# Kernel tuning notes

Measured on AMD Instinct MI355X. Metric: run time of the kernel, lower is better.

## Reference

```python
import jax, jax.numpy as jnp
from jax import lax
import numpy as np

TAG_NAMES = ["O", "B-MAT", "I-MAT", "B-PRO", "I-PRO", "B-APL", "I-APL", "B-SMT", "I-SMT", "B-CMT", "I-CMT", "B-DSC", "I-DSC"]
IMP = -100.0


def _init_crf_params(key):
    # torchcrf initializes uniform(-0.1, 0.1); CRF_NEW then clamps invalid
    # BIO transitions to -100 per define_invalid_crf_transitions/init_crf_transitions.
    K = len(TAG_NAMES)
    k1, k2, k3 = jax.random.split(key, 3)
    start = np.array(jax.random.uniform(k1, (K,), minval=-0.1, maxval=0.1), dtype=np.float32)
    end = np.array(jax.random.uniform(k2, (K,), minval=-0.1, maxval=0.1), dtype=np.float32)
    trans = np.array(jax.random.uniform(k3, (K, K), minval=-0.1, maxval=0.1), dtype=np.float32)
    pref = [t[0] for t in TAG_NAMES]
    ent = [t.split('-')[1] if '-' in t else '' for t in TAG_NAMES]
    for i in range(K):
        if pref[i] in ('B', 'I'):  # invalid begin/end for BIO
            start[i] = IMP
            end[i] = IMP
    for i in range(K):
        for j in range(K):
            # invalid_transitions_position: O -> I  (B->P, I->P are empty sets)
            if pref[i] == 'O' and pref[j] == 'I':
                trans[i, j] = IMP
            # invalid_transitions_tags: B->I, I->I across different entity types
            if pref[i] in ('B', 'I') and pref[j] == 'I' and ent[i] != ent[j]:
                trans[i, j] = IMP
    return jnp.asarray(start), jnp.asarray(end), jnp.asarray(trans)


def setup_inputs() -> dict:
    key = jax.random.key(0)
    k_em, k_tag, k_p = jax.random.split(key, 3)
    B, T, K = 4096, 512, len(TAG_NAMES)
    emissions = jax.random.normal(k_em, (B, T, K), dtype=jnp.float32)
    tags = jax.random.randint(k_tag, (B, T), 0, K, dtype=jnp.int64)
    mask = jnp.ones((B, T), dtype=bool)
    start_transitions, end_transitions, transitions = _init_crf_params(k_p)
    return {"emissions": emissions, "tags": tags, "mask": mask,
            "start_transitions": start_transitions,
            "end_transitions": end_transitions,
            "transitions": transitions}


def reference(emissions, tags, mask, start_transitions, end_transitions, transitions):
    # torchcrf CRF.forward with batch_first=True, reduction='sum':
    # returns sum over batch of log p(tags | emissions).
    B, T, K = emissions.shape
    maskf = mask.astype(emissions.dtype)

    # ---- numerator: score of the given tag path ----
    emit = jnp.take_along_axis(emissions, tags[..., None], axis=2)[..., 0]  # [B,T]
    trans = transitions[tags[:, :-1], tags[:, 1:]]                           # [B,T-1]
    num = start_transitions[tags[:, 0]] + emit[:, 0]
    num = num + jnp.sum((trans + emit[:, 1:]) * maskf[:, 1:], axis=1)
    seq_ends = jnp.sum(mask.astype(jnp.int32), axis=1) - 1                   # [B]
    last_tags = tags[jnp.arange(B), seq_ends]
    num = num + end_transitions[last_tags]

    # ---- denominator: log partition via forward-algorithm scan over time ----
    em_t = jnp.swapaxes(emissions, 0, 1)   # [T,B,K]
    mask_t = jnp.swapaxes(mask, 0, 1)      # [T,B]
    score0 = start_transitions + em_t[0]   # [B,K]

    def step(score, xs):
        em, m = xs  # em: [B,K], m: [B]
        # broadcast: [B,K_from,1] + [K_from,K_to] + [B,1,K_to]
        nxt = jax.nn.logsumexp(score[:, :, None] + transitions[None] + em[:, None, :], axis=1)
        return jnp.where(m[:, None], nxt, score), None

    score, _ = lax.scan(step, score0, (em_t[1:], mask_t[1:]))
    denom = jax.nn.logsumexp(score + end_transitions, axis=1)  # [B]

    return jnp.sum(num - denom)
```

## Files before the change

kernel.cpp:

```cpp
#include <hip/hip_runtime.h>


typedef float  f4  __attribute__((ext_vector_type(4)));
typedef short  s4  __attribute__((ext_vector_type(4)));
typedef int    i2  __attribute__((ext_vector_type(2)));

__device__ __forceinline__ unsigned pack_bf16(float x, float y) {
  return __builtin_amdgcn_perm(__float_as_uint(y) + 0x8000u,
                               __float_as_uint(x) + 0x8000u, 0x07060302u);
}

__device__ __forceinline__ void gll16(const void* g, void* l) {
  __builtin_amdgcn_global_load_lds(
      (const __attribute__((address_space(1))) void*)g,
      (__attribute__((address_space(3))) void*)l, 16, 0, 0);
}

#define VMWAIT(N) do { asm volatile("s_waitcnt vmcnt(" #N ")" ::: "memory"); \
                       __builtin_amdgcn_sched_barrier(0); } while (0)
#define SB0() __builtin_amdgcn_sched_barrier(0)

__global__ void __launch_bounds__(128, 1)
crf_main(const float* __restrict__ em,
         const int*   __restrict__ tags,
         const float* __restrict__ startT,
         const float* __restrict__ endT,
         const float* __restrict__ trans,
         float* __restrict__ partial)
{
  __shared__ __align__(16) float emST[2][3][4096];
  __shared__ __align__(16) int   tagST[2][3][256];
  __shared__ float ldsT[256];
  __shared__ float ldsS[16], ldsE[16];
  __shared__ float pFa[256];
  __shared__ float lsF[16], numF[16], resB[16];
  __shared__ int   tag255[16];

  const int tid = threadIdx.x;
  for (int i = tid; i < 169; i += 128) {
    const int r_ = i / 13, c_ = i - r_ * 13;
    ldsT[r_ * 16 + c_] = trans[i];
  }
  if (tid < 13) ldsS[tid] = startT[tid];
  if (tid >= 16 && tid < 29) ldsE[tid - 16] = endT[tid - 16];
  __syncthreads();

  const int lane = tid & 63;
  const int n    = lane & 15;
  const int q    = lane >> 4;
  const bool is_fwd = (tid < 64);
  const int  w   = is_fwd ? 0 : 1;
  const int  seq = blockIdx.x * 16 + n;
  const int loadBase = (q < 3) ? 4 * q : 9;
  const int lo       = (q < 3) ? 4 * q : 12;
  const unsigned span = (q < 3) ? 3u : 0u;
  const float* emL = em   + (size_t)seq * 6656 + loadBase;
  const int*   tgL = tags + (size_t)seq * 512 + 4 * q;
  const int   lofs = lane * 4;

  s4 afrag;
  {
    float av[4];
#pragma unroll
    for (int i = 0; i < 4; ++i) {
      const int kk = 4 * q + i;
      av[i] = (kk < 13 && n < 13)
            ? __expf(is_fwd ? ldsT[kk * 16 + n] : ldsT[n * 16 + kk]) : 0.0f;
    }
    i2 ai = { (int)pack_bf16(av[0], av[1]), (int)pack_bf16(av[2], av[3]) };
    afrag = __builtin_bit_cast(s4, ai);
  }

  f4 D;
#pragma unroll
  for (int r = 0; r < 4; ++r) {
    const int m = 4 * q + r;
    D[r] = (m < 13) ? __expf(is_fwd ? ldsS[m] : ldsE[m]) : 0.0f;
  }

  float logscale = 0.0f, em_acc = 0.0f, trans_acc = 0.0f;
  float sDs0 = 0, sDs1 = 0, sDs2 = 0, sDs3 = 0;
  float start_t0 = 0.0f;
  int tg_hi = 0, tg_lo = 0, tg511 = 0;
  int4 tG[4];

#define TGV(k) ((((k) & 3) == 0) ? tG[(k) >> 2].x : (((k) & 3) == 1) ? tG[(k) >> 2].y \
              : (((k) & 3) == 2) ? tG[(k) >> 2].z : tG[(k) >> 2].w)

#define STAGE(SL, TC) do {                                               \
    float* eb_ = &emST[w][SL][0];                                        \
    const float* gp_ = emL + (size_t)(TC) * 13;                          \
    _Pragma("unroll")                                                    \
    for (int k_ = 0; k_ < 16; ++k_)                                      \
      gll16(gp_ + (size_t)k_ * 13, eb_ + k_ * 256);                      \
    gll16(tgL + (TC), &tagST[w][SL][0]);                                 \
  } while (0)

#define LDTAGS(SL) do {                                                  \
    _Pragma("unroll")                                                    \
    for (int g_ = 0; g_ < 4; ++g_)                                       \
      tG[g_] = *(const int4*)&tagST[w][SL][(g_ * 16 + n) * 4];           \
  } while (0)

#define RENORM4() do {                                                  \
    float cm_ = fmaxf(fmaxf(Ds0, Ds1), fmaxf(Ds2, Ds3));                \
    cm_ = fmaxf(cm_, __shfl_xor(cm_, 16, 64));                          \
    cm_ = fmaxf(cm_, __shfl_xor(cm_, 32, 64));                          \
    const float rc_ = __builtin_amdgcn_rcpf(cm_);                       \
    Ds0 *= rc_; Ds1 *= rc_; Ds2 *= rc_; Ds3 *= rc_;                     \
    logscale += __logf(cm_);                                            \
  } while (0)

#define CORE(EM4, RN, TGVv) do {                                        \
    const float e0 = __expf((q == 3) ? (EM4).w : (EM4).x);              \
    const float e1 = __expf((EM4).y);                                   \
    const float e2 = __expf((EM4).z);                                   \
    const float e3 = __expf((EM4).w);                                   \
    Ds0 = D[0] * e0; Ds1 = D[1] * e1; Ds2 = D[2] * e2; Ds3 = D[3] * e3; \
    if (RN) RENORM4();                                                  \
    {                                                                   \
      const unsigned ur_ = (unsigned)((TGVv) - lo);                     \
      const int rr_ = (TGVv) - loadBase;                                \
      const float s01_ = (rr_ & 1) ? (EM4).y : (EM4).x;                 \
      const float s23_ = (rr_ & 1) ? (EM4).w : (EM4).z;                 \
      const float sv_  = (rr_ & 2) ? s23_ : s01_;                       \
      em_acc += (ur_ <= span) ? sv_ : 0.0f;                             \
    }                                                                   \
    {                                                                   \
      i2 bi_ = { (int)pack_bf16(Ds0, Ds1), (int)pack_bf16(Ds2, Ds3) };  \
      s4 bf_ = __builtin_bit_cast(s4, bi_);                             \
      D = __builtin_amdgcn_mfma_f32_16x16x16bf16_1k(                    \
              afrag, bf_, (f4){0.f, 0.f, 0.f, 0.f}, 0, 0, 0);           \
    }                                                                   \
  } while (0)

#define PROCF(SL, FIRST, LAST) do {                                     \
    _Pragma("unroll")                                                   \
    for (int k = 0; k < 16; ++k) {                                      \
      const int tgv = TGV(k);                                           \
      if (FIRST && k == 0) start_t0 = ldsS[tgv];                        \
      else {                                                            \
        const int pv = (k == 0) ? tg_hi : TGV(k - 1);                   \
        trans_acc += ldsT[pv * 16 + tgv];                               \
      }                                                                 \
      const f4 em4 = *(const f4*)&emST[w][SL][k * 256 + lofs];          \
      float Ds0, Ds1, Ds2, Ds3;                                         \
      CORE(em4, (k == 7 || k == 15), tgv);                              \
      if (LAST && k == 15) { sDs0 = Ds0; sDs1 = Ds1; sDs2 = Ds2; sDs3 = Ds3; } \
    }                                                                   \
    tg_hi = TGV(15);                                                    \
  } while (0)

#define PROCB(SL, FIRST) do {                                           \
    if (FIRST) tg511 = TGV(15);                                         \
    else       trans_acc += ldsT[TGV(15) * 16 + tg_lo];                 \
    _Pragma("unroll")                                                   \
    for (int kk = 0; kk < 16; ++kk) {                                   \
      const int k = 15 - kk;                                            \
      const int tgv = TGV(k);                                           \
      if (k > 0) trans_acc += ldsT[TGV(k - 1) * 16 + tgv];              \
      const f4 em4 = *(const f4*)&emST[w][SL][k * 256 + lofs];          \
      float Ds0, Ds1, Ds2, Ds3;                                         \
      CORE(em4, (k == 8 || k == 0), tgv);                               \
    }                                                                   \
    tg_lo = TGV(0);                                                     \
  } while (0)

  if (is_fwd) {
    STAGE(0, 0); STAGE(1, 16); STAGE(2, 32);
    VMWAIT(34); LDTAGS(0); PROCF(0, true, false); SB0(); STAGE(0, 48);
#pragma unroll 1
    for (int c = 1; c <= 10; c += 3) {
      VMWAIT(34); LDTAGS(1); PROCF(1, false, false); SB0(); STAGE(1, 16 * c + 48);
      VMWAIT(34); LDTAGS(2); PROCF(2, false, false); SB0(); STAGE(2, 16 * c + 64);
      VMWAIT(34); LDTAGS(0); PROCF(0, false, false); SB0(); STAGE(0, 16 * c + 80);
    }
    VMWAIT(34); LDTAGS(1); PROCF(1, false, false);
    VMWAIT(17); LDTAGS(2); PROCF(2, false, false);
    VMWAIT(0);  LDTAGS(0); PROCF(0, false, true);
    float emr = em_acc + __shfl_xor(em_acc, 16, 64);
    emr += __shfl_xor(emr, 32, 64);
    if (q == 0) {
      lsF[n]    = logscale;
      numF[n]   = start_t0 + emr + trans_acc;
      tag255[n] = tg_hi;
    }
    *(f4*)&pFa[n * 16 + 4 * q] = (f4){sDs0, sDs1, sDs2, sDs3};
  } else {
    STAGE(0, 496); STAGE(1, 480); STAGE(2, 464);
    VMWAIT(34); LDTAGS(0); PROCB(0, true); SB0(); STAGE(0, 448);
#pragma unroll 1
    for (int c = 1; c <= 10; c += 3) {
      VMWAIT(34); LDTAGS(1); PROCB(1, false); SB0(); STAGE(1, 448 - 16 * c);
      VMWAIT(34); LDTAGS(2); PROCB(2, false); SB0(); STAGE(2, 432 - 16 * c);
      VMWAIT(34); LDTAGS(0); PROCB(0, false); SB0(); STAGE(0, 416 - 16 * c);
    }
    VMWAIT(34); LDTAGS(1); PROCB(1, false);
    VMWAIT(17); LDTAGS(2); PROCB(2, false);
    VMWAIT(0);  LDTAGS(0); PROCB(0, false);
  }

  __syncthreads();

  if (!is_fwd) {
    const f4 al = *(const f4*)&pFa[n * 16 + 4 * q];
    float z = al[0] * D[0] + al[1] * D[1] + al[2] * D[2] + al[3] * D[3];
    z += __shfl_xor(z, 16, 64);
    z += __shfl_xor(z, 32, 64);
    float emr = em_acc + __shfl_xor(em_acc, 16, 64);
    emr += __shfl_xor(emr, 32, 64);
    const float denom = lsF[n] + logscale + __logf(z);
    const float num   = numF[n] + emr + trans_acc
                      + ldsT[tag255[n] * 16 + tg_lo]
                      + ldsE[tg511];
    if (q == 0) resB[n] = num - denom;
  }
  __syncthreads();
  if (tid == 0) {
    float s = 0.0f;
#pragma unroll
    for (int i = 0; i < 16; ++i) s += resB[i];
    partial[blockIdx.x] = s;
  }

#undef TGV
#undef STAGE
#undef LDTAGS
#undef RENORM4
#undef CORE
#undef PROCF
#undef PROCB
}

__global__ void __launch_bounds__(256)
crf_reduce(const float* __restrict__ part, float* __restrict__ out, int n)
{
  float v = 0.0f;
  for (int i = threadIdx.x; i < n; i += 256) v += part[i];
#pragma unroll
  for (int off = 32; off > 0; off >>= 1) v += __shfl_down(v, off);
  __shared__ float w[4];
  if ((threadIdx.x & 63) == 0) w[threadIdx.x >> 6] = v;
  __syncthreads();
  if (threadIdx.x == 0) out[0] = (w[0] + w[1]) + (w[2] + w[3]);
}

extern "C" void kernel_launch(void* const* d_in, const int* in_sizes, int n_in,
                              void* d_out, int out_size, void* d_ws, size_t ws_size,
                              hipStream_t stream) {
  const float* em   = (const float*)d_in[0];
  const int*   tags = (const int*)d_in[1];
  const float* st   = (const float*)d_in[3];
  const float* en   = (const float*)d_in[4];
  const float* tr   = (const float*)d_in[5];
  float* part = (float*)d_ws;

  crf_main<<<256, 128, 0, stream>>>(em, tags, st, en, tr, part);
  crf_reduce<<<1, 256, 0, stream>>>(part, (float*)d_out, 256);
}
```

Baseline: 194.3 us.

## Split batch into smaller blocks of four sequences with register-staged chunk loads

Each block now handles 4 sequences instead of 16 and the grid grows fourfold, with launch bounds allowing two blocks per CU. The aim is more resident waves per CU to hide the latency of the serial forward/backward recurrence. Emissions and tags now come in as 32-step chunks through registers into a double-buffered LDS area, replacing the triple-buffered direct global-to-LDS loads. The 16-column MFMA now holds each sequence four times, so per-sequence math is redundant. LDS emission reads become scalar with a 13-float stride.

```diff
diff --git a/kernel.cpp b/kernel.cpp
--- a/kernel.cpp
+++ b/kernel.cpp
@@ -5,22 +5,14 @@
 typedef short  s4  __attribute__((ext_vector_type(4)));
 typedef int    i2  __attribute__((ext_vector_type(2)));
 
+#define SB0() __builtin_amdgcn_sched_barrier(0)
+
 __device__ __forceinline__ unsigned pack_bf16(float x, float y) {
   return __builtin_amdgcn_perm(__float_as_uint(y) + 0x8000u,
                                __float_as_uint(x) + 0x8000u, 0x07060302u);
 }
 
-__device__ __forceinline__ void gll16(const void* g, void* l) {
-  __builtin_amdgcn_global_load_lds(
-      (const __attribute__((address_space(1))) void*)g,
-      (__attribute__((address_space(3))) void*)l, 16, 0, 0);
-}
-
-#define VMWAIT(N) do { asm volatile("s_waitcnt vmcnt(" #N ")" ::: "memory"); \
-                       __builtin_amdgcn_sched_barrier(0); } while (0)
-#define SB0() __builtin_amdgcn_sched_barrier(0)
-
-__global__ void __launch_bounds__(128, 1)
+__global__ void __launch_bounds__(128, 2)
 crf_main(const float* __restrict__ em,
          const int*   __restrict__ tags,
          const float* __restrict__ startT,
@@ -28,12 +20,12 @@
          const float* __restrict__ trans,
          float* __restrict__ partial)
 {
-  __shared__ __align__(16) float emST[2][3][4096];
-  __shared__ __align__(16) int   tagST[2][3][256];
+  __shared__ __align__(16) float emLds[2][2][4 * 420];
+  __shared__ __align__(16) int   tgLds[2][2][4 * 36];
   __shared__ float ldsT[256];
   __shared__ float ldsS[16], ldsE[16];
   __shared__ float pFa[256];
-  __shared__ float lsF[16], numF[16], resB[16];
+  __shared__ float lsF[16], numF[16], resB[4];
   __shared__ int   tag255[16];
 
   const int tid = threadIdx.x;
@@ -50,13 +42,19 @@
   const int q    = lane >> 4;
   const bool is_fwd = (tid < 64);
   const int  w   = is_fwd ? 0 : 1;
-  const int  seq = blockIdx.x * 16 + n;
+  const int  sl  = n & 3;
   const int loadBase = (q < 3) ? 4 * q : 9;
   const int lo       = (q < 3) ? 4 * q : 12;
   const unsigned span = (q < 3) ? 3u : 0u;
-  const float* emL = em   + (size_t)seq * 6656 + loadBase;
-  const int*   tgL = tags + (size_t)seq * 512 + 4 * q;
-  const int   lofs = lane * 4;
+  const int lb = loadBase;
+
+  const int ls = lane >> 4;
+  const int lp = lane & 15;
+  const int ts   = lane >> 3;
+  const int tg_g = lane & 7;
+  const int seqBlock = blockIdx.x * 4;
+  const float* emBase = em   + (size_t)(seqBlock + ls) * 6656;
+  const int*   tgBase = tags + (size_t)(seqBlock + ts) * 512;
 
   s4 afrag;
   {
@@ -82,24 +80,35 @@
   float sDs0 = 0, sDs1 = 0, sDs2 = 0, sDs3 = 0;
   float start_t0 = 0.0f;
   int tg_hi = 0, tg_lo = 0, tg511 = 0;
-  int4 tG[4];
+  int4 tG[8];
+  f4   rr[7];
+  int4 rt;
 
 #define TGV(k) ((((k) & 3) == 0) ? tG[(k) >> 2].x : (((k) & 3) == 1) ? tG[(k) >> 2].y \
               : (((k) & 3) == 2) ? tG[(k) >> 2].z : tG[(k) >> 2].w)
 
-#define STAGE(SL, TC) do {                                               \
-    float* eb_ = &emST[w][SL][0];                                        \
-    const float* gp_ = emL + (size_t)(TC) * 13;                          \
-    _Pragma("unroll")                                                    \
-    for (int k_ = 0; k_ < 16; ++k_)                                      \
-      gll16(gp_ + (size_t)k_ * 13, eb_ + k_ * 256);                      \
-    gll16(tgL + (TC), &tagST[w][SL][0]);                                 \
-  } while (0)
-
-#define LDTAGS(SL) do {                                                  \
-    _Pragma("unroll")                                                    \
-    for (int g_ = 0; g_ < 4; ++g_)                                       \
-      tG[g_] = *(const int4*)&tagST[w][SL][(g_ * 16 + n) * 4];           \
+#define LOADCH(T0) do {                                                 \
+    const float* gb_ = emBase + (size_t)(T0) * 13;                      \
+    _Pragma("unroll")                                                   \
+    for (int j_ = 0; j_ < 6; ++j_)                                      \
+      rr[j_] = *(const f4*)(gb_ + j_ * 64 + lp * 4);                    \
+    if (lp < 8) rr[6] = *(const f4*)(gb_ + 384 + lp * 4);               \
+    if (lane < 32) rt = *(const int4*)(tgBase + (T0) + tg_g * 4);       \
+  } while (0)
+
+#define WRCH(SL) do {                                                   \
+    float* wb_ = &emLds[w][SL][ls * 420];                               \
+    _Pragma("unroll")                                                   \
+    for (int j_ = 0; j_ < 6; ++j_)                                      \
+      *(f4*)(wb_ + j_ * 64 + lp * 4) = rr[j_];                          \
+    if (lp < 8) *(f4*)(wb_ + 384 + lp * 4) = rr[6];                     \
+    if (lane < 32) *(int4*)&tgLds[w][SL][ts * 36 + tg_g * 4] = rt;      \
+  } while (0)
+
+#define LDTAGS(SL) do {                                                 \
+    _Pragma("unroll")                                                   \
+    for (int g_ = 0; g_ < 8; ++g_)                                      \
+      tG[g_] = *(const int4*)&tgLds[w][SL][sl * 36 + g_ * 4];           \
   } while (0)
 
 #define RENORM4() do {                                                  \
@@ -134,50 +143,56 @@
     }                                                                   \
   } while (0)
 
+#define EMRD(SL, k, EM4) do {                                           \
+    const float* eb_ = &emLds[w][SL][sl * 420 + lb];                    \
+    (EM4).x = eb_[(k) * 13];     (EM4).y = eb_[(k) * 13 + 1];           \
+    (EM4).z = eb_[(k) * 13 + 2]; (EM4).w = eb_[(k) * 13 + 3];           \
+  } while (0)
+
 #define PROCF(SL, FIRST, LAST) do {                                     \
     _Pragma("unroll")                                                   \
-    for (int k = 0; k < 16; ++k) {                                      \
+    for (int k = 0; k < 32; ++k) {                                      \
       const int tgv = TGV(k);                                           \
-      if (FIRST && k == 0) start_t0 = ldsS[tgv];                        \
+      if ((FIRST) && k == 0) start_t0 = ldsS[tgv];                      \
       else {                                                            \
         const int pv = (k == 0) ? tg_hi : TGV(k - 1);                   \
         trans_acc += ldsT[pv * 16 + tgv];                               \
       }                                                                 \
-      const f4 em4 = *(const f4*)&emST[w][SL][k * 256 + lofs];          \
+      f4 em4; EMRD(SL, k, em4);                                         \
       float Ds0, Ds1, Ds2, Ds3;                                         \
-      CORE(em4, (k == 7 || k == 15), tgv);                              \
-      if (LAST && k == 15) { sDs0 = Ds0; sDs1 = Ds1; sDs2 = Ds2; sDs3 = Ds3; } \
-    }                                                                   \
-    tg_hi = TGV(15);                                                    \
+      CORE(em4, ((k & 7) == 7), tgv);                                   \
+      if ((LAST) && k == 31) { sDs0 = Ds0; sDs1 = Ds1; sDs2 = Ds2; sDs3 = Ds3; } \
+    }                                                                   \
+    tg_hi = TGV(31);                                                    \
   } while (0)
 
 #define PROCB(SL, FIRST) do {                                           \
-    if (FIRST) tg511 = TGV(15);                                         \
-    else       trans_acc += ldsT[TGV(15) * 16 + tg_lo];                 \
-    _Pragma("unroll")                                                   \
-    for (int kk = 0; kk < 16; ++kk) {                                   \
-      const int k = 15 - kk;                                            \
+    if (FIRST) tg511 = TGV(31);                                         \
+    else       trans_acc += ldsT[TGV(31) * 16 + tg_lo];                 \
+    _Pragma("unroll")                                                   \
+    for (int kk = 0; kk < 32; ++kk) {                                   \
+      const int k = 31 - kk;                                            \
       const int tgv = TGV(k);                                           \
       if (k > 0) trans_acc += ldsT[TGV(k - 1) * 16 + tgv];              \
-      const f4 em4 = *(const f4*)&emST[w][SL][k * 256 + lofs];          \
+      f4 em4; EMRD(SL, k, em4);                                         \
       float Ds0, Ds1, Ds2, Ds3;                                         \
-      CORE(em4, (k == 8 || k == 0), tgv);                               \
+      CORE(em4, ((k & 7) == 0), tgv);                                   \
     }                                                                   \
     tg_lo = TGV(0);                                                     \
   } while (0)
 
   if (is_fwd) {
-    STAGE(0, 0); STAGE(1, 16); STAGE(2, 32);
-    VMWAIT(34); LDTAGS(0); PROCF(0, true, false); SB0(); STAGE(0, 48);
+    LOADCH(0); SB0(); WRCH(0); SB0();
 #pragma unroll 1
-    for (int c = 1; c <= 10; c += 3) {
-      VMWAIT(34); LDTAGS(1); PROCF(1, false, false); SB0(); STAGE(1, 16 * c + 48);
-      VMWAIT(34); LDTAGS(2); PROCF(2, false, false); SB0(); STAGE(2, 16 * c + 64);
-      VMWAIT(34); LDTAGS(0); PROCF(0, false, false); SB0(); STAGE(0, 16 * c + 80);
-    }
-    VMWAIT(34); LDTAGS(1); PROCF(1, false, false);
-    VMWAIT(17); LDTAGS(2); PROCF(2, false, false);
-    VMWAIT(0);  LDTAGS(0); PROCF(0, false, true);
+    for (int c = 0; c < 8; ++c) {
+      if (c < 7) LOADCH(32 * c + 32);
+      SB0();
+      LDTAGS(c & 1);
+      PROCF(c & 1, c == 0, c == 7);
+      SB0();
+      if (c < 7) WRCH((c + 1) & 1);
+      SB0();
+    }
     float emr = em_acc + __shfl_xor(em_acc, 16, 64);
     emr += __shfl_xor(emr, 32, 64);
     if (q == 0) {
@@ -187,17 +202,17 @@
     }
     *(f4*)&pFa[n * 16 + 4 * q] = (f4){sDs0, sDs1, sDs2, sDs3};
   } else {
-    STAGE(0, 496); STAGE(1, 480); STAGE(2, 464);
-    VMWAIT(34); LDTAGS(0); PROCB(0, true); SB0(); STAGE(0, 448);
+    LOADCH(480); SB0(); WRCH(0); SB0();
 #pragma unroll 1
-    for (int c = 1; c <= 10; c += 3) {
-      VMWAIT(34); LDTAGS(1); PROCB(1, false); SB0(); STAGE(1, 448 - 16 * c);
-      VMWAIT(34); LDTAGS(2); PROCB(2, false); SB0(); STAGE(2, 432 - 16 * c);
-      VMWAIT(34); LDTAGS(0); PROCB(0, false); SB0(); STAGE(0, 416 - 16 * c);
-    }
-    VMWAIT(34); LDTAGS(1); PROCB(1, false);
-    VMWAIT(17); LDTAGS(2); PROCB(2, false);
-    VMWAIT(0);  LDTAGS(0); PROCB(0, false);
+    for (int c = 0; c < 8; ++c) {
+      if (c < 7) LOADCH(448 - 32 * c);
+      SB0();
+      LDTAGS(c & 1);
+      PROCB(c & 1, c == 0);
+      SB0();
+      if (c < 7) WRCH((c + 1) & 1);
+      SB0();
+    }
   }
 
   __syncthreads();
@@ -213,21 +228,21 @@
     const float num   = numF[n] + emr + trans_acc
                       + ldsT[tag255[n] * 16 + tg_lo]
                       + ldsE[tg511];
-    if (q == 0) resB[n] = num - denom;
+    if (q == 0 && n < 4) resB[n] = num - denom;
   }
   __syncthreads();
   if (tid == 0) {
-    float s = 0.0f;
-#pragma unroll
-    for (int i = 0; i < 16; ++i) s += resB[i];
+    float s = (resB[0] + resB[1]) + (resB[2] + resB[3]);
     partial[blockIdx.x] = s;
   }
 
 #undef TGV
-#undef STAGE
+#undef LOADCH
+#undef WRCH
 #undef LDTAGS
 #undef RENORM4
 #undef CORE
+#undef EMRD
 #undef PROCF
 #undef PROCB
 }
@@ -255,6 +270,6 @@
   const float* tr   = (const float*)d_in[5];
   float* part = (float*)d_ws;
 
-  crf_main<<<256, 128, 0, stream>>>(em, tags, st, en, tr, part);
-  crf_reduce<<<1, 256, 0, stream>>>(part, (float*)d_out, 256);
-}
+  crf_main<<<1024, 128, 0, stream>>>(em, tags, st, en, tr, part);
+  crf_reduce<<<1, 256, 0, stream>>>(part, (float*)d_out, 1024);
+}
```

New measurement: 247.1 us. 1.27x slower.
